# Performance work log

Measured on AMD Instinct MI355X. Metric: run time of the kernel, lower is better.

The kernel has to match this reference:

```python
import jax, jax.numpy as jnp
import numpy as np

SEQ, BATCH, IN, HID = 2048, 128, 128, 256
ALPHA = 0.1  # dt/tau = 10/100


def setup_inputs() -> dict:
    key = jax.random.key(0)
    ks = jax.random.split(key, 5)
    x = jax.random.normal(ks[0], (SEQ, BATCH, IN), dtype=jnp.float32)
    h0 = jnp.zeros((BATCH, HID), dtype=jnp.float32)
    W_in = jax.random.normal(ks[1], (HID, IN), dtype=jnp.float32) / np.sqrt(IN)
    b_in = jax.random.normal(ks[2], (HID,), dtype=jnp.float32) * 0.01
    W_h = jax.random.normal(ks[3], (HID, HID), dtype=jnp.float32) / np.sqrt(HID)
    b_h = jax.random.normal(ks[4], (HID,), dtype=jnp.float32) * 0.01
    return {"x": x, "h0": h0, "W_in": W_in, "b_in": b_in, "W_h": W_h, "b_h": b_h}


def reference(x, h0, W_in, b_in, W_h, b_h):
    # Precompute input projection for all timesteps in one GEMM: (S,B,H)
    xin = jnp.einsum('sbi,hi->sbh', x, W_in) + b_in

    def step(h, xin_t):
        h_new = jax.nn.relu(xin_t + h @ W_h.T + b_h)
        h = h * (1.0 - ALPHA) + h_new * ALPHA
        return h, h

    h_final, outputs = jax.lax.scan(step, h0, xin)
    return outputs, h_final
```

## Files before the change

kernel.cpp:

```cpp
#include <hip/hip_runtime.h>

#define SEQ   2048
#define BATCH 128
#define INDIM 128
#define HID   256
#define BH    (BATCH * HID)
#define SB    (SEQ * BATCH)

template <int CTRL>
__device__ __forceinline__ float dpp_mov_f32(float v) {
  return __int_as_float(
      __builtin_amdgcn_update_dpp(0, __float_as_int(v), CTRL, 0xF, 0xF, false));
}
__device__ __forceinline__ float sum8(float v) {
  v += dpp_mov_f32<0xB1>(v);
  v += dpp_mov_f32<0x4E>(v);
  v += dpp_mov_f32<0x141>(v);
  return v;
}

#define TM 128
#define TN 128
#define KC 64

__global__ __launch_bounds__(256, 2) void xin_gemm(
    const float* __restrict__ x, const float* __restrict__ W_in,
    const float* __restrict__ b_in, const float* __restrict__ b_h,
    float* __restrict__ out) {
  __shared__ __align__(16) float As[TM * KC];
  __shared__ __align__(16) float Bs[TN * KC];

  const int tid = threadIdx.x;
  const int bm  = blockIdx.x >> 1;
  const int bn  = blockIdx.x & 1;
  const int mg  = tid & 15;
  const int ng  = tid >> 4;
  const int rotA = 4 * (mg & 7);
  const int rotB = 4 * (ng & 7);

  const float4* xg = (const float4*)(x + (size_t)bm * TM * INDIM);
  const float4* wg = (const float4*)(W_in + (size_t)bn * TN * INDIM);

  float acc[8][8] = {};

  for (int h = 0; h < 2; ++h) {
#pragma unroll
    for (int s = 0; s < 8; ++s) {
      const int id = tid + 256 * s;
      const int r  = id >> 4;
      const int c4 = id & 15;
      const int rc = (4 * c4 + 4 * ((r >> 3) & 7)) & (KC - 1);
      float4 va = xg[(size_t)r * 32 + c4 + 16 * h];
      *(float4*)(As + r * KC + rc) = va;
      float4 vb = wg[(size_t)r * 32 + c4 + 16 * h];
      *(float4*)(Bs + r * KC + rc) = vb;
    }
    __syncthreads();

#pragma unroll 4
    for (int k4 = 0; k4 < KC / 4; ++k4) {
      const int ca = (4 * k4 + rotA) & (KC - 1);
      const int cb = (4 * k4 + rotB) & (KC - 1);
      float4 a[8], bb[8];
#pragma unroll
      for (int i = 0; i < 8; ++i)
        a[i] = *(const float4*)(As + (8 * mg + i) * KC + ca);
#pragma unroll
      for (int j = 0; j < 8; ++j)
        bb[j] = *(const float4*)(Bs + (8 * ng + j) * KC + cb);
#pragma unroll
      for (int i = 0; i < 8; ++i)
#pragma unroll
        for (int j = 0; j < 8; ++j) {
          acc[i][j] = fmaf(a[i].x, bb[j].x, acc[i][j]);
          acc[i][j] = fmaf(a[i].y, bb[j].y, acc[i][j]);
          acc[i][j] = fmaf(a[i].z, bb[j].z, acc[i][j]);
          acc[i][j] = fmaf(a[i].w, bb[j].w, acc[i][j]);
        }
    }
    __syncthreads();
  }

  const int row0 = bm * TM + 8 * mg;
  const int n0   = bn * TN + 8 * ng;
  float bi[8];
#pragma unroll
  for (int j = 0; j < 8; ++j) bi[j] = b_in[n0 + j] + b_h[n0 + j];
#pragma unroll
  for (int i = 0; i < 8; ++i) {
    float4 lo = make_float4(acc[i][0] + bi[0], acc[i][1] + bi[1],
                            acc[i][2] + bi[2], acc[i][3] + bi[3]);
    float4 hi = make_float4(acc[i][4] + bi[4], acc[i][5] + bi[5],
                            acc[i][6] + bi[6], acc[i][7] + bi[7]);
    float* o = out + (size_t)(row0 + i) * HID + n0;
    *(float4*)o       = lo;
    *(float4*)(o + 4) = hi;
  }
}

#define PADS 36

__global__ __launch_bounds__(256, 1) void ctrnn_rec(
    const float* __restrict__ h0, const float* __restrict__ W_h,
    float* out) {
  __shared__ __align__(16) float hs[2][8 * PADS];

  const int b   = blockIdx.x;
  const int tid = threadIdx.x;
  const int q   = tid & 7;
  const int g   = tid >> 3;

  float w[8][32];
#pragma unroll
  for (int i = 0; i < 8; ++i) {
    const float4* wg = (const float4*)(W_h + (size_t)(8 * g + i) * HID + 32 * q);
#pragma unroll
    for (int k4 = 0; k4 < 8; ++k4) {
      float4 v = wg[k4];
      w[i][4*k4+0] = v.x; w[i][4*k4+1] = v.y;
      w[i][4*k4+2] = v.z; w[i][4*k4+3] = v.w;
    }
  }

  float hr[8];
  {
    float4 h40 = *(const float4*)(h0 + (size_t)b * HID + 8 * g);
    float4 h41 = *(const float4*)(h0 + (size_t)b * HID + 8 * g + 4);
    hr[0]=h40.x; hr[1]=h40.y; hr[2]=h40.z; hr[3]=h40.w;
    hr[4]=h41.x; hr[5]=h41.y; hr[6]=h41.z; hr[7]=h41.w;
  }

  float* const wslot0 = &hs[0][PADS * (g >> 2) + 8 * (g & 3)];
  float* const wslot1 = &hs[1][PADS * (g >> 2) + 8 * (g & 3)];
  const float* const rb0 = &hs[0][PADS * q];
  const float* const rb1 = &hs[1][PADS * q];

  if (q == 0) {
    *(float4*)wslot0       = make_float4(hr[0], hr[1], hr[2], hr[3]);
    *(float4*)(wslot0 + 4) = make_float4(hr[4], hr[5], hr[6], hr[7]);
  }

  float* const io = out + (size_t)b * HID + 8 * g;
  float4 xA0 = ((const float4*)io)[0];
  float4 xA1 = ((const float4*)io)[1];
  float4 xB0 = ((const float4*)(io + (size_t)BH))[0];
  float4 xB1 = ((const float4*)(io + (size_t)BH))[1];

  __syncthreads();

  auto step = [&](int t, const float* rbuf, float* wslot) {
    float4 xC0 = xA0, xC1 = xA1;
    if (t + 2 < SEQ) {
      xC0 = ((const float4*)(io + (size_t)(t + 2) * BH))[0];
      xC1 = ((const float4*)(io + (size_t)(t + 2) * BH))[1];
    }

    const float4* hv = (const float4*)rbuf;
    float a[8] = {0.f, 0.f, 0.f, 0.f, 0.f, 0.f, 0.f, 0.f};
#pragma unroll
    for (int k4 = 0; k4 < 8; ++k4) {
      float4 v = hv[k4];
#pragma unroll
      for (int i = 0; i < 8; ++i) {
        a[i] = fmaf(w[i][4*k4+0], v.x, a[i]);
        a[i] = fmaf(w[i][4*k4+1], v.y, a[i]);
        a[i] = fmaf(w[i][4*k4+2], v.z, a[i]);
        a[i] = fmaf(w[i][4*k4+3], v.w, a[i]);
      }
    }
#pragma unroll
    for (int i = 0; i < 8; ++i) a[i] = sum8(a[i]);

    const float xi[8] = {xA0.x, xA0.y, xA0.z, xA0.w,
                         xA1.x, xA1.y, xA1.z, xA1.w};
#pragma unroll
    for (int i = 0; i < 8; ++i)
      hr[i] = fmaf(0.1f, fmaxf(a[i] + xi[i], 0.f), 0.9f * hr[i]);

    if (q == 0) {
      float4 lo = make_float4(hr[0], hr[1], hr[2], hr[3]);
      float4 hi = make_float4(hr[4], hr[5], hr[6], hr[7]);
      *(float4*)wslot       = lo;
      *(float4*)(wslot + 4) = hi;
      float* o = io + (size_t)t * BH;
      *(float4*)o       = lo;
      *(float4*)(o + 4) = hi;
    }
    xA0 = xB0; xA1 = xB1; xB0 = xC0; xB1 = xC1;
    __syncthreads();
  };

  for (int t = 0; t < SEQ; t += 2) {
    step(t, rb0, wslot1);
    step(t + 1, rb1, wslot0);
  }

  if (q == 0) {
    float* o = io + (size_t)SEQ * BH;
    *(float4*)o       = make_float4(hr[0], hr[1], hr[2], hr[3]);
    *(float4*)(o + 4) = make_float4(hr[4], hr[5], hr[6], hr[7]);
  }
}

extern "C" void kernel_launch(void* const* d_in, const int* in_sizes, int n_in,
                              void* d_out, int out_size, void* d_ws, size_t ws_size,
                              hipStream_t stream) {
  const float* x    = (const float*)d_in[0];
  const float* h0   = (const float*)d_in[1];
  const float* W_in = (const float*)d_in[2];
  const float* b_in = (const float*)d_in[3];
  const float* W_h  = (const float*)d_in[4];
  const float* b_h  = (const float*)d_in[5];
  float* out = (float*)d_out;

  xin_gemm<<<(SB / TM) * (HID / TN), 256, 0, stream>>>(x, W_in, b_in, b_h, out);
  ctrnn_rec<<<BATCH, 256, 0, stream>>>(h0, W_h, out);
}
```

Measured before the change: 2.839 ms.

## Split recurrent dot products across 16 lanes with 512-thread blocks

The recurrent kernel now uses 512 threads per batch row, each lane holding 8x16 weights instead of 8x32, so the serial FMA chain per timestep is halved. Reductions are widened to 16 lanes with an extra DPP step, and two lanes per group apply the update and write four outputs each. The full __syncthreads is replaced by an LDS-only waitcnt plus s_barrier to shorten the per-step barrier. The trade-off is twice as many waves to synchronise per step, an extra reduction stage, and a 16-lane DPP row-broadcast step that has to combine correctly within a row.

```diff
diff --git a/kernel.cpp b/kernel.cpp
--- a/kernel.cpp
+++ b/kernel.cpp
@@ -12,11 +12,18 @@
   return __int_as_float(
       __builtin_amdgcn_update_dpp(0, __float_as_int(v), CTRL, 0xF, 0xF, false));
 }
-__device__ __forceinline__ float sum8(float v) {
+__device__ __forceinline__ float sum16(float v) {
   v += dpp_mov_f32<0xB1>(v);
   v += dpp_mov_f32<0x4E>(v);
   v += dpp_mov_f32<0x141>(v);
+  v += dpp_mov_f32<0x140>(v);
   return v;
+}
+
+__device__ __forceinline__ void block_sync_lds() {
+  asm volatile("s_waitcnt lgkmcnt(0)" ::: "memory");
+  __builtin_amdgcn_s_barrier();
+  asm volatile("" ::: "memory");
 }
 
 #define TM 128
@@ -98,67 +105,55 @@
   }
 }
 
-#define PADS 36
-
-__global__ __launch_bounds__(256, 1) void ctrnn_rec(
+#define SPAD 20
+
+__global__ __launch_bounds__(512, 2) void ctrnn_rec(
     const float* __restrict__ h0, const float* __restrict__ W_h,
     float* out) {
-  __shared__ __align__(16) float hs[2][8 * PADS];
-
-  const int b   = blockIdx.x;
-  const int tid = threadIdx.x;
-  const int q   = tid & 7;
-  const int g   = tid >> 3;
-
-  float w[8][32];
+  __shared__ __align__(16) float hs[2][16 * SPAD];
+
+  const int b    = blockIdx.x;
+  const int tid  = threadIdx.x;
+  const int q    = tid & 15;
+  const int g    = tid >> 4;
+  const int half = q & 1;
+
+  float w[8][16];
 #pragma unroll
   for (int i = 0; i < 8; ++i) {
-    const float4* wg = (const float4*)(W_h + (size_t)(8 * g + i) * HID + 32 * q);
-#pragma unroll
-    for (int k4 = 0; k4 < 8; ++k4) {
-      float4 v = wg[k4];
+    const float4* wgp = (const float4*)(W_h + (size_t)(8 * g + i) * HID + 16 * q);
+#pragma unroll
+    for (int k4 = 0; k4 < 4; ++k4) {
+      float4 v = wgp[k4];
       w[i][4*k4+0] = v.x; w[i][4*k4+1] = v.y;
       w[i][4*k4+2] = v.z; w[i][4*k4+3] = v.w;
     }
   }
 
-  float hr[8];
-  {
-    float4 h40 = *(const float4*)(h0 + (size_t)b * HID + 8 * g);
-    float4 h41 = *(const float4*)(h0 + (size_t)b * HID + 8 * g + 4);
-    hr[0]=h40.x; hr[1]=h40.y; hr[2]=h40.z; hr[3]=h40.w;
-    hr[4]=h41.x; hr[5]=h41.y; hr[6]=h41.z; hr[7]=h41.w;
-  }
-
-  float* const wslot0 = &hs[0][PADS * (g >> 2) + 8 * (g & 3)];
-  float* const wslot1 = &hs[1][PADS * (g >> 2) + 8 * (g & 3)];
-  const float* const rb0 = &hs[0][PADS * q];
-  const float* const rb1 = &hs[1][PADS * q];
-
-  if (q == 0) {
-    *(float4*)wslot0       = make_float4(hr[0], hr[1], hr[2], hr[3]);
-    *(float4*)(wslot0 + 4) = make_float4(hr[4], hr[5], hr[6], hr[7]);
-  }
-
-  float* const io = out + (size_t)b * HID + 8 * g;
-  float4 xA0 = ((const float4*)io)[0];
-  float4 xA1 = ((const float4*)io)[1];
-  float4 xB0 = ((const float4*)(io + (size_t)BH))[0];
-  float4 xB1 = ((const float4*)(io + (size_t)BH))[1];
-
-  __syncthreads();
-
-  auto step = [&](int t, const float* rbuf, float* wslot) {
-    float4 xC0 = xA0, xC1 = xA1;
-    if (t + 2 < SEQ) {
-      xC0 = ((const float4*)(io + (size_t)(t + 2) * BH))[0];
-      xC1 = ((const float4*)(io + (size_t)(t + 2) * BH))[1];
-    }
-
-    const float4* hv = (const float4*)rbuf;
+  float4 h4 = *(const float4*)(h0 + (size_t)b * HID + 8 * g + 4 * half);
+  float hr[4] = {h4.x, h4.y, h4.z, h4.w};
+
+  float* const wr0 = &hs[0][SPAD * (g >> 1) + 8 * (g & 1) + 4 * half];
+  float* const wr1 = &hs[1][SPAD * (g >> 1) + 8 * (g & 1) + 4 * half];
+  const float* const rd0 = &hs[0][SPAD * q];
+  const float* const rd1 = &hs[1][SPAD * q];
+
+  if (q < 2) *(float4*)wr0 = h4;
+
+  float* const io = out + (size_t)b * HID + 8 * g + 4 * half;
+  float4 xA = *(const float4*)io;
+  float4 xB = *(const float4*)(io + (size_t)BH);
+
+  block_sync_lds();
+
+  auto step = [&](int t, const float* rd, float* wr) {
+    float4 xC = xA;
+    if (t + 2 < SEQ) xC = *(const float4*)(io + (size_t)(t + 2) * BH);
+
+    const float4* hv = (const float4*)rd;
     float a[8] = {0.f, 0.f, 0.f, 0.f, 0.f, 0.f, 0.f, 0.f};
 #pragma unroll
-    for (int k4 = 0; k4 < 8; ++k4) {
+    for (int k4 = 0; k4 < 4; ++k4) {
       float4 v = hv[k4];
 #pragma unroll
       for (int i = 0; i < 8; ++i) {
@@ -169,37 +164,34 @@
       }
     }
 #pragma unroll
-    for (int i = 0; i < 8; ++i) a[i] = sum8(a[i]);
-
-    const float xi[8] = {xA0.x, xA0.y, xA0.z, xA0.w,
-                         xA1.x, xA1.y, xA1.z, xA1.w};
-#pragma unroll
-    for (int i = 0; i < 8; ++i)
-      hr[i] = fmaf(0.1f, fmaxf(a[i] + xi[i], 0.f), 0.9f * hr[i]);
-
-    if (q == 0) {
-      float4 lo = make_float4(hr[0], hr[1], hr[2], hr[3]);
-      float4 hi = make_float4(hr[4], hr[5], hr[6], hr[7]);
-      *(float4*)wslot       = lo;
-      *(float4*)(wslot + 4) = hi;
-      float* o = io + (size_t)t * BH;
-      *(float4*)o       = lo;
-      *(float4*)(o + 4) = hi;
-    }
-    xA0 = xB0; xA1 = xB1; xB0 = xC0; xB1 = xC1;
-    __syncthreads();
+    for (int i = 0; i < 8; ++i) a[i] = sum16(a[i]);
+
+    const float s0 = half ? a[4] : a[0];
+    const float s1 = half ? a[5] : a[1];
+    const float s2 = half ? a[6] : a[2];
+    const float s3 = half ? a[7] : a[3];
+
+    hr[0] = fmaf(0.1f, fmaxf(s0 + xA.x, 0.f), 0.9f * hr[0]);
+    hr[1] = fmaf(0.1f, fmaxf(s1 + xA.y, 0.f), 0.9f * hr[1]);
+    hr[2] = fmaf(0.1f, fmaxf(s2 + xA.z, 0.f), 0.9f * hr[2]);
+    hr[3] = fmaf(0.1f, fmaxf(s3 + xA.w, 0.f), 0.9f * hr[3]);
+
+    if (q < 2) {
+      float4 hw = make_float4(hr[0], hr[1], hr[2], hr[3]);
+      *(float4*)wr = hw;
+      *(float4*)(io + (size_t)t * BH) = hw;
+    }
+    xA = xB; xB = xC;
+    block_sync_lds();
   };
 
   for (int t = 0; t < SEQ; t += 2) {
-    step(t, rb0, wslot1);
-    step(t + 1, rb1, wslot0);
-  }
-
-  if (q == 0) {
-    float* o = io + (size_t)SEQ * BH;
-    *(float4*)o       = make_float4(hr[0], hr[1], hr[2], hr[3]);
-    *(float4*)(o + 4) = make_float4(hr[4], hr[5], hr[6], hr[7]);
-  }
+    step(t, rd0, wr1);
+    step(t + 1, rd1, wr0);
+  }
+
+  if (q < 2)
+    *(float4*)(io + (size_t)SEQ * BH) = make_float4(hr[0], hr[1], hr[2], hr[3]);
 }
 
 extern "C" void kernel_launch(void* const* d_in, const int* in_sizes, int n_in,
@@ -214,5 +206,5 @@
   float* out = (float*)d_out;
 
   xin_gemm<<<(SB / TM) * (HID / TN), 256, 0, stream>>>(x, W_in, b_in, b_h, out);
-  ctrnn_rec<<<BATCH, 256, 0, stream>>>(h0, W_h, out);
-}
+  ctrnn_rec<<<BATCH, 512, 0, stream>>>(h0, W_h, out);
+}
```

New measurement: 2.423 ms. 1.17x faster.
